# Performance work log

Hardware: AMD Instinct MI355X
Metric: run time of the kernel (lower is better)

The kernel has to match this reference:

```python
import jax, jax.numpy as jnp
import numpy as np

B, S, D_MODEL, N_HEADS = 2, 2048, 2048, 16
D_K = D_MODEL // N_HEADS
MAX_SEQ_LEN = 4096


def _rope_tables(seq_len, d_k):
    # matches RotaryPositionalEmbedding buffers
    inv_freq = 1.0 / (10000.0 ** (jnp.arange(0, d_k, 2, dtype=jnp.float32) / d_k))
    pos = jnp.arange(seq_len, dtype=jnp.float32)
    freqs = pos[:, None] * inv_freq[None, :]  # [S, d_k/2]
    return jnp.cos(freqs), jnp.sin(freqs)


def _apply_rope(x, cos, sin):
    # x: [B, H, S, d_k]; cos/sin: [S, d_k/2] -> broadcast [1,1,S,d_k/2]
    cos = cos[None, None, :, :]
    sin = sin[None, None, :, :]
    x_even = x[..., ::2]
    x_odd = x[..., 1::2]
    r_even = x_even * cos - x_odd * sin
    r_odd = x_even * sin + x_odd * cos
    return jnp.stack([r_even, r_odd], axis=-1).reshape(x.shape)


def setup_inputs() -> dict:
    key = jax.random.key(0)
    ks = jax.random.split(key, 5)
    scale = 1.0 / np.sqrt(D_MODEL)
    return {
        "x": jax.random.normal(ks[0], (B, S, D_MODEL), jnp.float32),
        "wq_w": jax.random.normal(ks[1], (D_MODEL, D_MODEL), jnp.float32) * scale,
        "wq_b": jnp.zeros((D_MODEL,), jnp.float32),
        "wk_w": jax.random.normal(ks[2], (D_MODEL, D_MODEL), jnp.float32) * scale,
        "wk_b": jnp.zeros((D_MODEL,), jnp.float32),
        "wv_w": jax.random.normal(ks[3], (D_MODEL, D_MODEL), jnp.float32) * scale,
        "wv_b": jnp.zeros((D_MODEL,), jnp.float32),
        "wo_w": jax.random.normal(ks[4], (D_MODEL, D_MODEL), jnp.float32) * scale,
        "wo_b": jnp.zeros((D_MODEL,), jnp.float32),
    }


def reference(x, wq_w, wq_b, wk_w, wk_b, wv_w, wv_b, wo_w, wo_b):
    b, s, _ = x.shape
    # QKV projections (torch Linear: x @ W.T + b), split heads -> [B, H, S, d_k]
    def proj(w, bias):
        y = jnp.einsum('bsd,ed->bse', x, w) + bias
        return y.reshape(b, s, N_HEADS, D_K).transpose(0, 2, 1, 3)

    q = proj(wq_w, wq_b)
    k = proj(wk_w, wk_b)
    v = proj(wv_w, wv_b)

    cos, sin = _rope_tables(s, D_K)
    q = _apply_rope(q, cos, sin)
    k = _apply_rope(k, cos, sin)

    # causal SDPA
    scale = 1.0 / np.sqrt(D_K).astype(np.float32)
    scores = jnp.einsum('bhqd,bhkd->bhqk', q, k) * scale
    causal = jnp.tril(jnp.ones((s, s), dtype=bool))
    scores = jnp.where(causal[None, None, :, :], scores, jnp.float32(-jnp.inf))
    attn = jax.nn.softmax(scores, axis=-1)
    out = jnp.einsum('bhqk,bhkd->bhqd', attn, v)

    out = out.transpose(0, 2, 1, 3).reshape(b, s, D_MODEL)
    return jnp.einsum('bsd,ed->bse', out, wo_w) + wo_b
```

## Files before the change

### kernel.cpp

```cpp
#include <hip/hip_runtime.h>


#define DMODEL 2048
#define SEQ    2048
#define NHEAD  16
#define DKH    128
#define NBATCH 2
#define MTOK   (NBATCH*SEQ)

typedef float  f32x4  __attribute__((ext_vector_type(4)));
typedef __bf16 bf16x8 __attribute__((ext_vector_type(8)));
typedef unsigned short      u16;
typedef unsigned short      u16x4 __attribute__((ext_vector_type(4)));

#if __has_builtin(__builtin_amdgcn_exp2f)
#define EXP2F __builtin_amdgcn_exp2f
#else
#define EXP2F exp2f
#endif

__device__ __forceinline__ float b2f(u16 u) {
    union { unsigned i; float f; } x; x.i = ((unsigned)u) << 16; return x.f;
}
__device__ __forceinline__ u16 f2bf(float f) {
    union { float f; unsigned i; } x; x.f = f;
    unsigned r = x.i + 0x7fffu + ((x.i >> 16) & 1u);
    return (u16)(r >> 16);
}

__device__ __forceinline__ void load_lds16(const void* g, void* l) {
    __builtin_amdgcn_global_load_lds(
        (const __attribute__((address_space(1))) void*)g,
        (__attribute__((address_space(3))) void*)l, 16, 0, 0);
}

#define WAITVM(N) asm volatile("s_waitcnt vmcnt(" #N ")" ::: "memory")

struct CastArgs {
    const float* src[5];
    u16*         dst[5];
    int          n4[5];
};
__global__ void cast_all_kernel(CastArgs a) {
    int j = blockIdx.y;
    int i = blockIdx.x * blockDim.x + threadIdx.x;
    if (i >= a.n4[j]) return;
    float4 f = ((const float4*)a.src[j])[i];
    uint2 o;
    o.x = (unsigned)f2bf(f.x) | ((unsigned)f2bf(f.y) << 16);
    o.y = (unsigned)f2bf(f.z) | ((unsigned)f2bf(f.w) << 16);
    ((uint2*)a.dst[j])[i] = o;
}

__global__ __launch_bounds__(512, 2) void gemm_qkv256(
    const u16* __restrict__ A, const u16* __restrict__ W,
    const float* __restrict__ qb, const float* __restrict__ kb,
    const float* __restrict__ vb,
    u16* __restrict__ QB, u16* __restrict__ KB, u16* __restrict__ VT)
{
    __shared__ __align__(16) u16 AS[4][8192];
    __shared__ __align__(16) u16 BS[4][8192];

    const int tid  = threadIdx.x;
    const int lane = tid & 63;
    const int w    = tid >> 6;
    const int wm   = w >> 2, wn = w & 3;
    const int quad = lane >> 4, l16 = lane & 15;

    const int xcd = blockIdx.x & 7, loc = blockIdx.x >> 3;
    const int rt  = loc / 3, cl2 = loc - rt * 3;
    const int row0 = rt * 256;
    const int col0 = (xcd * 3 + cl2) * 256;

    const int srow = lane >> 2;
    const int csrc = ((lane & 3) - ((lane >> 3) & 3)) & 3;
    const int rpos = (l16 >> 1) & 3;

    f32x4 acc[8][4] = {};
    bf16x8 af[4], bfr[4];

#define QSTAGE_A(t) { const int k0_ = (t) * 32; u16* S_ = AS[(t) & 3];            \
    load_lds16(A + (size_t)(row0 +       w * 16 + srow) * 2048 + k0_ + csrc * 8,  \
               (void*)(S_ + w * 512));                                            \
    load_lds16(A + (size_t)(row0 + 128 + w * 16 + srow) * 2048 + k0_ + csrc * 8,  \
               (void*)(S_ + 4096 + w * 512)); }
#define QSTAGE_B(t) { const int k0_ = (t) * 32; u16* S_ = BS[(t) & 3];            \
    load_lds16(W + (size_t)(col0 +       w * 16 + srow) * 2048 + k0_ + csrc * 8,  \
               (void*)(S_ + w * 512));                                            \
    load_lds16(W + (size_t)(col0 + 128 + w * 16 + srow) * 2048 + k0_ + csrc * 8,  \
               (void*)(S_ + 4096 + w * 512)); }

#define QDS_A(Sl, ph) _Pragma("unroll") for (int i = 0; i < 4; ++i) {             \
        int row_ = wm * 128 + ((ph) * 4 + i) * 16 + l16;                          \
        af[i] = *(const bf16x8*)((Sl) + row_ * 32 + ((quad + rpos) & 3) * 8); }
#define QDS_B(Sl) _Pragma("unroll") for (int ni = 0; ni < 4; ++ni) {              \
        int row_ = wn * 64 + ni * 16 + l16;                                       \
        bfr[ni] = *(const bf16x8*)((Sl) + row_ * 32 + ((quad + rpos) & 3) * 8); }

#define QMFMA(ph)                                                                 \
    __builtin_amdgcn_sched_barrier(0);                                            \
    __builtin_amdgcn_s_barrier();                                                 \
    asm volatile("s_waitcnt lgkmcnt(0)" ::: "memory");                            \
    __builtin_amdgcn_sched_barrier(0);                                            \
    __builtin_amdgcn_s_setprio(1);                                                \
    _Pragma("unroll") for (int i = 0; i < 4; ++i)                                 \
    _Pragma("unroll") for (int ni = 0; ni < 4; ++ni)                              \
        acc[(ph) * 4 + i][ni] = __builtin_amdgcn_mfma_f32_16x16x32_bf16(          \
            af[i], bfr[ni], acc[(ph) * 4 + i][ni], 0, 0, 0);                      \
    __builtin_amdgcn_s_setprio(0);                                                \
    __builtin_amdgcn_sched_barrier(0);                                            \
    __builtin_amdgcn_s_barrier();

    QSTAGE_A(0); QSTAGE_B(0);
    QSTAGE_A(1); QSTAGE_B(1);
    QSTAGE_A(2); QSTAGE_B(2);
    WAITVM(8);
    __builtin_amdgcn_s_barrier();

    for (int t = 0; t < 61; ++t) {
        const u16* Asl = AS[t & 3];
        const u16* Bsl = BS[t & 3];
        QDS_A(Asl, 0); QDS_B(Bsl);
        QSTAGE_A(t + 3);
        QMFMA(0);
        QDS_A(Asl, 1);
        QSTAGE_B(t + 3);
        WAITVM(8);
        QMFMA(1);
    }
    {
        const u16* Asl = AS[61 & 3]; const u16* Bsl = BS[61 & 3];
        QDS_A(Asl, 0); QDS_B(Bsl); QMFMA(0);
        QDS_A(Asl, 1); WAITVM(4);  QMFMA(1);
    }
    {
        const u16* Asl = AS[62 & 3]; const u16* Bsl = BS[62 & 3];
        QDS_A(Asl, 0); QDS_B(Bsl); QMFMA(0);
        QDS_A(Asl, 1); WAITVM(0);  QMFMA(1);
    }
    {
        const u16* Asl = AS[63 & 3]; const u16* Bsl = BS[63 & 3];
        QDS_A(Asl, 0); QDS_B(Bsl); QMFMA(0);
        QDS_A(Asl, 1);             QMFMA(1);
    }
#undef QSTAGE_A
#undef QSTAGE_B
#undef QDS_A
#undef QDS_B
#undef QMFMA

    const int sect = col0 >> 11;
    if (sect == 2) {
#pragma unroll
        for (int mi = 0; mi < 8; ++mi) {
#pragma unroll
            for (int ni = 0; ni < 4; ++ni) {
                int colv = (col0 & 2047) + wn * 64 + ni * 16 + l16;
                float bv = vb[colv];
                int rowb = row0 + wm * 128 + mi * 16 + quad * 4;
                int bb = rowb >> 11, s = rowb & 2047;
                u16x4 pk;
#pragma unroll
                for (int r = 0; r < 4; ++r) pk[r] = f2bf(acc[mi][ni][r] + bv);
                *(u16x4*)(VT + (size_t)(bb * 2048 + colv) * 2048 + s) = pk;
            }
        }
    } else {
        const float* bias = sect ? kb : qb;
        u16* dst          = sect ? KB : QB;
#pragma unroll
        for (int mi = 0; mi < 8; ++mi) {
#pragma unroll
            for (int ni = 0; ni < 4; ++ni) {
                int col = (col0 & 2047) + wn * 64 + ni * 16 + l16;
                float bv = bias[col];
#pragma unroll
                for (int r = 0; r < 4; ++r) {
                    int row = row0 + wm * 128 + mi * 16 + quad * 4 + r;
                    dst[(size_t)row * 2048 + col] = f2bf(acc[mi][ni][r] + bv);
                }
            }
        }
    }
}

__global__ __launch_bounds__(512, 2) void gemm_o_pipe(
    const u16* __restrict__ A, const u16* __restrict__ W,
    const float* __restrict__ bias, float* __restrict__ FO)
{
    constexpr int NT = 32;

    __shared__ __align__(16) u16 AS[3][128 * 64];
    __shared__ __align__(16) u16 BS[3][256 * 64];

    const int tid  = threadIdx.x;
    const int lane = tid & 63;
    const int w    = tid >> 6;
    const int wm   = w >> 2, wn = w & 3;
    const int quad = lane >> 4, l16 = lane & 15;

    const int xcd = blockIdx.x & 7, loc = blockIdx.x >> 3;
    const int row0 = (xcd * 4 + (loc & 3)) * 128;
    const int col0 = (loc >> 2) * 256;

    const int rl = lane >> 3;
    const int cg = (lane & 7) ^ rl;

    f32x4 acc[4][4] = {};
    bf16x8 af[4], bfr[4];

#define STAGE_A(slot, j, k0)                                                       \
    load_lds16(A + (size_t)(row0 + (j) * 64 + w * 8 + rl) * 2048 + (k0) + cg * 8,  \
               (void*)((slot) + ((j) * 8 + w) * 512))
#define STAGE_B(slot, j, k0)                                                       \
    load_lds16(W + (size_t)(col0 + (j) * 64 + w * 8 + rl) * 2048 + (k0) + cg * 8,  \
               (void*)((slot) + ((j) * 8 + w) * 512))

#define DS_FRAGS(slotA, slotB, ks)                                          \
    {                                                                       \
        _Pragma("unroll") for (int mi = 0; mi < 4; ++mi) {                  \
            int r  = wm * 64 + mi * 16 + l16;                               \
            int cc = ((ks) * 4 + quad) ^ (r & 7);                           \
            af[mi] = *(const bf16x8*)((slotA) + r * 64 + cc * 8);           \
        }                                                                   \
        _Pragma("unroll") for (int ni = 0; ni < 4; ++ni) {                  \
            int r  = wn * 64 + ni * 16 + l16;                               \
            int cc = ((ks) * 4 + quad) ^ (r & 7);                           \
            bfr[ni] = *(const bf16x8*)((slotB) + r * 64 + cc * 8);          \
        }                                                                   \
    }

#define MFMA16()                                                            \
    __builtin_amdgcn_sched_barrier(0);                                      \
    __builtin_amdgcn_s_barrier();                                           \
    asm volatile("s_waitcnt lgkmcnt(0)" ::: "memory");                      \
    __builtin_amdgcn_sched_barrier(0);                                      \
    __builtin_amdgcn_s_setprio(1);                                          \
    _Pragma("unroll") for (int mi = 0; mi < 4; ++mi)                        \
        _Pragma("unroll") for (int ni = 0; ni < 4; ++ni)                    \
            acc[mi][ni] = __builtin_amdgcn_mfma_f32_16x16x32_bf16(          \
                af[mi], bfr[ni], acc[mi][ni], 0, 0, 0);                     \
    __builtin_amdgcn_s_setprio(0);                                          \
    __builtin_amdgcn_sched_barrier(0);                                      \
    __builtin_amdgcn_s_barrier();

    STAGE_A(AS[0], 0, 0);  STAGE_A(AS[0], 1, 0);
    STAGE_B(BS[0], 0, 0);  STAGE_B(BS[0], 1, 0);
    STAGE_B(BS[0], 2, 0);  STAGE_B(BS[0], 3, 0);
    STAGE_A(AS[1], 0, 64); STAGE_A(AS[1], 1, 64);
    STAGE_B(BS[1], 0, 64); STAGE_B(BS[1], 1, 64);
    STAGE_B(BS[1], 2, 64); STAGE_B(BS[1], 3, 64);
    WAITVM(6);
    __builtin_amdgcn_s_barrier();

    int sC = 0, sS = 2;
    for (int t = 0; t < NT - 2; ++t) {
        u16* Ac  = AS[sC]; u16* Bc  = BS[sC];
        u16* Asg = AS[sS]; u16* Bsg = BS[sS];
        const int k0s = (t + 2) * 64;
        DS_FRAGS(Ac, Bc, 0);
        STAGE_A(Asg, 0, k0s); STAGE_A(Asg, 1, k0s); STAGE_B(Bsg, 0, k0s);
        MFMA16();
        DS_FRAGS(Ac, Bc, 1);
        STAGE_B(Bsg, 1, k0s); STAGE_B(Bsg, 2, k0s); STAGE_B(Bsg, 3, k0s);
        WAITVM(6);
        MFMA16();
        sC = (sC == 2) ? 0 : sC + 1;
        sS = (sS == 2) ? 0 : sS + 1;
    }
    {
        u16* Ac = AS[sC]; u16* Bc = BS[sC];
        DS_FRAGS(Ac, Bc, 0); MFMA16();
        DS_FRAGS(Ac, Bc, 1); WAITVM(0); MFMA16();
        sC = (sC == 2) ? 0 : sC + 1;
    }
    {
        u16* Ac = AS[sC]; u16* Bc = BS[sC];
        DS_FRAGS(Ac, Bc, 0); MFMA16();
        DS_FRAGS(Ac, Bc, 1);
        asm volatile("s_waitcnt lgkmcnt(0)" ::: "memory");
        __builtin_amdgcn_sched_barrier(0);
#pragma unroll
        for (int mi = 0; mi < 4; ++mi)
#pragma unroll
            for (int ni = 0; ni < 4; ++ni)
                acc[mi][ni] = __builtin_amdgcn_mfma_f32_16x16x32_bf16(
                    af[mi], bfr[ni], acc[mi][ni], 0, 0, 0);
    }

#pragma unroll
    for (int mi = 0; mi < 4; ++mi) {
#pragma unroll
        for (int ni = 0; ni < 4; ++ni) {
            int col = col0 + wn * 64 + ni * 16 + l16;
            float bv = bias[col];
#pragma unroll
            for (int r = 0; r < 4; ++r) {
                int row = row0 + wm * 64 + mi * 16 + quad * 4 + r;
                FO[(size_t)row * DMODEL + col] = acc[mi][ni][r] + bv;
            }
        }
    }
#undef STAGE_A
#undef STAGE_B
#undef DS_FRAGS
#undef MFMA16
}

__global__ void rope_kernel(u16* __restrict__ Q, u16* __restrict__ Kt) {
    int idx = blockIdx.x * blockDim.x + threadIdx.x;
    u16* P      = blockIdx.y ? Kt : Q;
    float scale = blockIdx.y ? 1.0f : 0.12751743558f;
    int i   = idx & 63;
    int tok = idx >> 10;
    int s   = tok & (SEQ - 1);
    unsigned pr = *(const unsigned*)(P + 2 * (size_t)idx);
    float e = b2f((u16)(pr & 0xffff)), o = b2f((u16)(pr >> 16));
    float inv_freq = exp2f(-13.287712379549449f * (float)i * (1.0f / 64.0f));
    float ang = (float)s * inv_freq;
    float c, sn;
    sincosf(ang, &sn, &c);
    float re = (e * c - o * sn) * scale;
    float ro = (e * sn + o * c) * scale;
    *(unsigned*)(P + 2 * (size_t)idx) = (unsigned)f2bf(re) | ((unsigned)f2bf(ro) << 16);
}

__global__ __launch_bounds__(512, 4) void attn_kernel(
    const u16* __restrict__ Q, const u16* __restrict__ Kg,
    const u16* __restrict__ VTg, u16* __restrict__ Out)
{
    const int p  = blockIdx.x;
    const int bh = blockIdx.y;
    const int b  = bh >> 4, h = bh & 15;

    const int tid  = threadIdx.x;
    const int lane = tid & 63;
    const int w    = tid >> 6;
    const int half = w >> 2;
    const int wsub = w & 3;
    const int quad = lane >> 4, l16 = lane & 15;

    const int q_hi  = 31 - p;
    const int my_qt = half ? q_hi : p;
    const int q0    = my_qt * 64;

    __shared__ u16 Ks[64 * 128];
    __shared__ u16 Vt[128 * 64];
    __shared__ u16 Ps[8][16 * 72];

    bf16x8 qf[4];
    const u16* qrow = Q + (size_t)(b * SEQ + q0 + wsub * 16 + l16) * DMODEL + h * DKH;
#pragma unroll
    for (int ks = 0; ks < 4; ++ks) qf[ks] = *(const bf16x8*)(qrow + ks * 32 + quad * 8);

    f32x4 o[8] = {};
    float l_r[4] = { 0.f, 0.f, 0.f, 0.f };

    for (int kt = 0; kt <= q_hi; ++kt) {
        const int k0 = kt * 64;
#pragma unroll
        for (int i = 0; i < 2; ++i) {
            int cb = (i * 8 + w) * 64;
            int pc = cb + lane;
            int r  = pc >> 4;
            int cl = (pc & 15) ^ (r & 15);
            load_lds16(Kg + (size_t)(b * SEQ + k0 + r) * DMODEL + h * DKH + cl * 8,
                       (void*)(Ks + cb * 8));
        }
#pragma unroll
        for (int i = 0; i < 2; ++i) {
            int cb = (i * 8 + w) * 64;
            int pc = cb + lane;
            int r  = pc >> 3;
            int cl = (pc & 7) ^ (r & 7);
            load_lds16(VTg + (size_t)(b * 2048 + h * DKH + r) * SEQ + k0 + cl * 8,
                       (void*)(Vt + cb * 8));
        }
        __syncthreads();

        if (kt <= my_qt) {
            f32x4 sc[4] = {};
#pragma unroll
            for (int ks = 0; ks < 4; ++ks) {
#pragma unroll
                for (int nt = 0; nt < 4; ++nt) {
                    int r  = nt * 16 + l16;
                    int pc = (ks * 4 + quad) ^ (r & 15);
                    bf16x8 kf = *(const bf16x8*)(Ks + (r * 16 + pc) * 8);
                    sc[nt] = __builtin_amdgcn_mfma_f32_16x16x32_bf16(qf[ks], kf, sc[nt], 0, 0, 0);
                }
            }
            if (kt == my_qt) {
#pragma unroll
                for (int nt = 0; nt < 4; ++nt)
#pragma unroll
                    for (int r = 0; r < 4; ++r) {
                        int col = k0 + nt * 16 + l16;
                        int row = q0 + wsub * 16 + quad * 4 + r;
                        if (col > row) sc[nt][r] = -1e30f;
                    }
            }
#pragma unroll
            for (int nt = 0; nt < 4; ++nt)
#pragma unroll
                for (int r = 0; r < 4; ++r) {
                    float pv = EXP2F(sc[nt][r] - 32.0f);
                    l_r[r] += pv;
                    Ps[w][(quad * 4 + r) * 72 + nt * 16 + l16] = f2bf(pv);
                }
#pragma unroll
            for (int ks = 0; ks < 2; ++ks) {
                bf16x8 pf = *(const bf16x8*)(&Ps[w][l16 * 72 + ks * 32 + quad * 8]);
#pragma unroll
                for (int nt = 0; nt < 8; ++nt) {
                    int r  = nt * 16 + l16;
                    int pc = (ks * 4 + quad) ^ (r & 7);
                    bf16x8 vf = *(const bf16x8*)(Vt + r * 64 + pc * 8);
                    o[nt] = __builtin_amdgcn_mfma_f32_16x16x32_bf16(pf, vf, o[nt], 0, 0, 0);
                }
            }
        }
        __syncthreads();
    }

#pragma unroll
    for (int r = 0; r < 4; ++r) {
#pragma unroll
        for (int off = 1; off < 16; off <<= 1) l_r[r] += __shfl_xor(l_r[r], off);
        float inv = 1.0f / l_r[r];
        int row = q0 + wsub * 16 + quad * 4 + r;
#pragma unroll
        for (int nt = 0; nt < 8; ++nt)
            Out[(size_t)(b * SEQ + row) * DMODEL + h * DKH + nt * 16 + l16] = f2bf(o[nt][r] * inv);
    }
}

extern "C" void kernel_launch(void* const* d_in, const int* in_sizes, int n_in,
                              void* d_out, int out_size, void* d_ws, size_t ws_size,
                              hipStream_t stream)
{
    const float* x    = (const float*)d_in[0];
    const float* wq_w = (const float*)d_in[1];
    const float* wq_b = (const float*)d_in[2];
    const float* wk_w = (const float*)d_in[3];
    const float* wk_b = (const float*)d_in[4];
    const float* wv_w = (const float*)d_in[5];
    const float* wv_b = (const float*)d_in[6];
    const float* wo_w = (const float*)d_in[7];
    const float* wo_b = (const float*)d_in[8];
    float* out = (float*)d_out;

    char* ws = (char*)d_ws;
    u16* XB   = (u16*)(ws);
    u16* WQKV = (u16*)(ws + (16u << 20));
    u16* WOB  = (u16*)(ws + (40u << 20));
    u16* QB   = (u16*)(ws + (48u << 20));
    u16* KB   = (u16*)(ws + (64u << 20));
    u16* VTB  = (u16*)(ws + (80u << 20));

    CastArgs ca;
    ca.src[0] = x;    ca.dst[0] = XB;                         ca.n4[0] = (MTOK * DMODEL) / 4;
    ca.src[1] = wq_w; ca.dst[1] = WQKV;                       ca.n4[1] = (DMODEL * DMODEL) / 4;
    ca.src[2] = wk_w; ca.dst[2] = WQKV + DMODEL * DMODEL;     ca.n4[2] = (DMODEL * DMODEL) / 4;
    ca.src[3] = wv_w; ca.dst[3] = WQKV + 2 * DMODEL * DMODEL; ca.n4[3] = (DMODEL * DMODEL) / 4;
    ca.src[4] = wo_w; ca.dst[4] = WOB;                        ca.n4[4] = (DMODEL * DMODEL) / 4;
    cast_all_kernel<<<dim3(8192, 5), 256, 0, stream>>>(ca);

    gemm_qkv256<<<dim3(384), 512, 0, stream>>>(
        XB, WQKV, wq_b, wk_b, wv_b, QB, KB, VTB);

    rope_kernel<<<dim3((MTOK * NHEAD * 64) / 256, 2), 256, 0, stream>>>(QB, KB);

    attn_kernel<<<dim3(16, NBATCH * NHEAD), 512, 0, stream>>>(QB, KB, VTB, XB);

    gemm_o_pipe<<<dim3(256), 512, 0, stream>>>(XB, WOB, wo_b, out);
}
```

Measured before the change: 385.2 us.

## Restructure QKV GEMM to double-buffered BK=64 tiles with XOR-swizzled LDS

The QKV projection GEMM main loop moves from a 4-deep ring of K=32 slices to two buffers of K=64 tiles, with an XOR swizzle on LDS column groups in place of the old rotation scheme. Each iteration prefetches the next full tile, runs four MFMA phases over two k-substeps, then waits for all outstanding loads before a barrier. This halves the number of loop iterations and changes the bank-conflict pattern. In exchange, prefetch depth drops to one tile, so memory latency may be less well hidden, and the full vmcnt(0) wait at the end of each iteration may expose load latency.

```diff
diff --git a/kernel.cpp b/kernel.cpp
--- a/kernel.cpp
+++ b/kernel.cpp
@@ -58,8 +58,8 @@
     const float* __restrict__ vb,
     u16* __restrict__ QB, u16* __restrict__ KB, u16* __restrict__ VT)
 {
-    __shared__ __align__(16) u16 AS[4][8192];
-    __shared__ __align__(16) u16 BS[4][8192];
+    __shared__ __align__(16) u16 AS[2][256 * 64];
+    __shared__ __align__(16) u16 BS[2][256 * 64];
 
     const int tid  = threadIdx.x;
     const int lane = tid & 63;
@@ -68,86 +68,73 @@
     const int quad = lane >> 4, l16 = lane & 15;
 
     const int xcd = blockIdx.x & 7, loc = blockIdx.x >> 3;
-    const int rt  = loc / 3, cl2 = loc - rt * 3;
+    const int rt  = loc / 3, cl = loc - rt * 3;
     const int row0 = rt * 256;
-    const int col0 = (xcd * 3 + cl2) * 256;
-
-    const int srow = lane >> 2;
-    const int csrc = ((lane & 3) - ((lane >> 3) & 3)) & 3;
-    const int rpos = (l16 >> 1) & 3;
+    const int col0 = (xcd * 3 + cl) * 256;
+
+    const int rl = lane >> 3;
+    const int cg = (lane & 7) ^ rl;
 
     f32x4 acc[8][4] = {};
     bf16x8 af[4], bfr[4];
 
-#define QSTAGE_A(t) { const int k0_ = (t) * 32; u16* S_ = AS[(t) & 3];            \
-    load_lds16(A + (size_t)(row0 +       w * 16 + srow) * 2048 + k0_ + csrc * 8,  \
-               (void*)(S_ + w * 512));                                            \
-    load_lds16(A + (size_t)(row0 + 128 + w * 16 + srow) * 2048 + k0_ + csrc * 8,  \
-               (void*)(S_ + 4096 + w * 512)); }
-#define QSTAGE_B(t) { const int k0_ = (t) * 32; u16* S_ = BS[(t) & 3];            \
-    load_lds16(W + (size_t)(col0 +       w * 16 + srow) * 2048 + k0_ + csrc * 8,  \
-               (void*)(S_ + w * 512));                                            \
-    load_lds16(W + (size_t)(col0 + 128 + w * 16 + srow) * 2048 + k0_ + csrc * 8,  \
-               (void*)(S_ + 4096 + w * 512)); }
-
-#define QDS_A(Sl, ph) _Pragma("unroll") for (int i = 0; i < 4; ++i) {             \
-        int row_ = wm * 128 + ((ph) * 4 + i) * 16 + l16;                          \
-        af[i] = *(const bf16x8*)((Sl) + row_ * 32 + ((quad + rpos) & 3) * 8); }
-#define QDS_B(Sl) _Pragma("unroll") for (int ni = 0; ni < 4; ++ni) {              \
-        int row_ = wn * 64 + ni * 16 + l16;                                       \
-        bfr[ni] = *(const bf16x8*)((Sl) + row_ * 32 + ((quad + rpos) & 3) * 8); }
-
-#define QMFMA(ph)                                                                 \
-    __builtin_amdgcn_sched_barrier(0);                                            \
-    __builtin_amdgcn_s_barrier();                                                 \
-    asm volatile("s_waitcnt lgkmcnt(0)" ::: "memory");                            \
-    __builtin_amdgcn_sched_barrier(0);                                            \
-    __builtin_amdgcn_s_setprio(1);                                                \
-    _Pragma("unroll") for (int i = 0; i < 4; ++i)                                 \
-    _Pragma("unroll") for (int ni = 0; ni < 4; ++ni)                              \
-        acc[(ph) * 4 + i][ni] = __builtin_amdgcn_mfma_f32_16x16x32_bf16(          \
-            af[i], bfr[ni], acc[(ph) * 4 + i][ni], 0, 0, 0);                      \
-    __builtin_amdgcn_s_setprio(0);                                                \
-    __builtin_amdgcn_sched_barrier(0);                                            \
+#define STG(dst, src, b0, j, k0)                                                   \
+    load_lds16(src + (size_t)((b0) + (j) * 64 + w * 8 + rl) * 2048 + (k0) + cg * 8,\
+               (void*)((dst) + ((j) * 8 + w) * 512))
+#define STAGE_TILE(t) {                                                            \
+    const int k0_ = (t) * 64;                                                      \
+    u16* As_ = AS[(t) & 1]; u16* Bs_ = BS[(t) & 1];                                \
+    STG(As_, A, row0, 0, k0_); STG(As_, A, row0, 1, k0_);                          \
+    STG(As_, A, row0, 2, k0_); STG(As_, A, row0, 3, k0_);                          \
+    STG(Bs_, W, col0, 0, k0_); STG(Bs_, W, col0, 1, k0_);                          \
+    STG(Bs_, W, col0, 2, k0_); STG(Bs_, W, col0, 3, k0_); }
+
+#define QDS_A(Sl, mh, ks) _Pragma("unroll") for (int mi = 0; mi < 4; ++mi) {       \
+        int ra = wm * 128 + (mh) * 64 + mi * 16 + l16;                             \
+        int cc = ((ks) * 4 + quad) ^ (ra & 7);                                     \
+        af[mi] = *(const bf16x8*)((Sl) + ra * 64 + cc * 8); }
+#define QDS_B(Sl, ks) _Pragma("unroll") for (int ni = 0; ni < 4; ++ni) {           \
+        int rb = wn * 64 + ni * 16 + l16;                                          \
+        int cc = ((ks) * 4 + quad) ^ (rb & 7);                                     \
+        bfr[ni] = *(const bf16x8*)((Sl) + rb * 64 + cc * 8); }
+
+#define QPHASE(mh)                                                                 \
+    __builtin_amdgcn_sched_barrier(0);                                             \
+    __builtin_amdgcn_s_barrier();                                                  \
+    asm volatile("s_waitcnt lgkmcnt(0)" ::: "memory");                             \
+    __builtin_amdgcn_sched_barrier(0);                                             \
+    __builtin_amdgcn_s_setprio(1);                                                 \
+    _Pragma("unroll") for (int mi = 0; mi < 4; ++mi)                               \
+    _Pragma("unroll") for (int ni = 0; ni < 4; ++ni)                               \
+        acc[(mh) * 4 + mi][ni] = __builtin_amdgcn_mfma_f32_16x16x32_bf16(          \
+            af[mi], bfr[ni], acc[(mh) * 4 + mi][ni], 0, 0, 0);                     \
+    __builtin_amdgcn_s_setprio(0);                                                 \
+    __builtin_amdgcn_sched_barrier(0);
+
+    STAGE_TILE(0);
+    WAITVM(0);
     __builtin_amdgcn_s_barrier();
 
-    QSTAGE_A(0); QSTAGE_B(0);
-    QSTAGE_A(1); QSTAGE_B(1);
-    QSTAGE_A(2); QSTAGE_B(2);
-    WAITVM(8);
-    __builtin_amdgcn_s_barrier();
-
-    for (int t = 0; t < 61; ++t) {
-        const u16* Asl = AS[t & 3];
-        const u16* Bsl = BS[t & 3];
-        QDS_A(Asl, 0); QDS_B(Bsl);
-        QSTAGE_A(t + 3);
-        QMFMA(0);
-        QDS_A(Asl, 1);
-        QSTAGE_B(t + 3);
-        WAITVM(8);
-        QMFMA(1);
-    }
-    {
-        const u16* Asl = AS[61 & 3]; const u16* Bsl = BS[61 & 3];
-        QDS_A(Asl, 0); QDS_B(Bsl); QMFMA(0);
-        QDS_A(Asl, 1); WAITVM(4);  QMFMA(1);
-    }
-    {
-        const u16* Asl = AS[62 & 3]; const u16* Bsl = BS[62 & 3];
-        QDS_A(Asl, 0); QDS_B(Bsl); QMFMA(0);
-        QDS_A(Asl, 1); WAITVM(0);  QMFMA(1);
-    }
-    {
-        const u16* Asl = AS[63 & 3]; const u16* Bsl = BS[63 & 3];
-        QDS_A(Asl, 0); QDS_B(Bsl); QMFMA(0);
-        QDS_A(Asl, 1);             QMFMA(1);
-    }
-#undef QSTAGE_A
-#undef QSTAGE_B
+    for (int t = 0; t < 32; ++t) {
+        const u16* Asl = AS[t & 1];
+        const u16* Bsl = BS[t & 1];
+        if (t < 31) STAGE_TILE(t + 1);
+        QDS_A(Asl, 0, 0); QDS_B(Bsl, 0);
+        QPHASE(0); __builtin_amdgcn_s_barrier();
+        QDS_A(Asl, 1, 0);
+        QPHASE(1); __builtin_amdgcn_s_barrier();
+        QDS_A(Asl, 0, 1); QDS_B(Bsl, 1);
+        QPHASE(0); __builtin_amdgcn_s_barrier();
+        QDS_A(Asl, 1, 1);
+        QPHASE(1);
+        if (t < 31) { WAITVM(0); }
+        __builtin_amdgcn_s_barrier();
+    }
+#undef STG
+#undef STAGE_TILE
 #undef QDS_A
 #undef QDS_B
-#undef QMFMA
+#undef QPHASE
 
     const int sect = col0 >> 11;
     if (sect == 2) {
```

New measurement: 410.5 us. 1.07x slower.
